# Kernel tuning notes

Measured on AMD Instinct MI355X. Metric: run time of the kernel, lower is better.

Reference implementation:

```python
import jax, jax.numpy as jnp
import numpy as np

B, N, C, K, D = 32, 4096, 37, 100, 512   # images, rois, classes(incl bg), max dets/class, feat dim
C1 = C - 1
SCORE_TH, NMS_TH = 0.1, 0.4
BBOX_STDS = jnp.array([0.1, 0.1, 0.2, 0.2], jnp.float32)
HS, WS, SCALE = 960.0, 1280.0, 1.6  # scaled image height/width, resize scale


def setup_inputs() -> dict:
    key = jax.random.key(0)
    k1, k2, k3, k4 = jax.random.split(key, 4)
    u = jax.random.uniform(k1, (B, N, 4))
    x1 = u[..., 0] * (WS - 160.0)
    y1 = u[..., 1] * (HS - 160.0)
    w = u[..., 2] * 140.0 + 20.0
    h = u[..., 3] * 140.0 + 20.0
    boxes = jnp.stack([x1, y1, x1 + w, y1 + h], -1)          # [B,N,4] in scaled coords
    box_deltas = jax.random.normal(k2, (B, N, 4 * C)) * 0.5   # [B,N,4C]
    scores = jax.nn.softmax(jax.random.normal(k3, (B, N, C)) * 2.0, axis=-1)  # [B,N,C]
    roi_features = jax.random.normal(k4, (B, N, D))           # [B,N,D]
    im_info = jnp.tile(jnp.array([[HS, WS, SCALE]], jnp.float32), (B, 1))     # [B,3]
    return dict(boxes=boxes, box_deltas=box_deltas, scores=scores,
                roi_features=roi_features, im_info=im_info)


def _decode_clip(boxes, deltas, im_info):
    # bbox_transform_inv with normalize stds, then clip_boxes, then /scale.
    d = deltas.reshape(B, N, C, 4) * BBOX_STDS                # [B,N,C,4]
    w = boxes[..., 2] - boxes[..., 0] + 1.0
    h = boxes[..., 3] - boxes[..., 1] + 1.0
    cx = boxes[..., 0] + 0.5 * w
    cy = boxes[..., 1] + 0.5 * h
    pcx = d[..., 0] * w[..., None] + cx[..., None]
    pcy = d[..., 1] * h[..., None] + cy[..., None]
    pw = jnp.exp(d[..., 2]) * w[..., None]
    ph = jnp.exp(d[..., 3]) * h[..., None]
    hmax = im_info[:, 0][:, None, None] - 1.0
    wmax = im_info[:, 1][:, None, None] - 1.0
    x1 = jnp.clip(pcx - 0.5 * pw, 0.0, wmax)
    y1 = jnp.clip(pcy - 0.5 * ph, 0.0, hmax)
    x2 = jnp.clip(pcx + 0.5 * pw, 0.0, wmax)
    y2 = jnp.clip(pcy + 0.5 * ph, 0.0, hmax)
    pred = jnp.stack([x1, y1, x2, y2], -1)                    # [B,N,C,4]
    return pred / im_info[:, 2][:, None, None, None]


def _pairwise_iou(b):
    # b: [K,4] -> [K,K]
    area = (b[:, 2] - b[:, 0]) * (b[:, 3] - b[:, 1])
    lt = jnp.maximum(b[:, None, :2], b[None, :, :2])
    rb = jnp.minimum(b[:, None, 2:], b[None, :, 2:])
    wh = jnp.clip(rb - lt, 0.0)
    inter = wh[..., 0] * wh[..., 1]
    return inter / (area[:, None] + area[None, :] - inter + 1e-8)


def _nms_one_class(cls_boxes, cls_scores, feats):
    # cls_boxes [N,4], cls_scores [N], feats [N,D] -> det [K, 4+1+D]
    s = jnp.where(cls_scores > SCORE_TH, cls_scores, -1.0)
    vals, idx = jax.lax.top_k(s, K)                           # sorted desc == torch.sort(desc)
    b = cls_boxes[idx]                                        # [K,4]
    ious = _pairwise_iou(b)                                   # [K,K]
    valid = vals > SCORE_TH
    rng = jnp.arange(K)

    def body(i, keep):
        sup = (ious[i] > NMS_TH) & (rng > i) & keep[i]
        return keep & ~sup

    keep = jax.lax.fori_loop(0, K, body, valid)               # greedy NMS, fixed size
    det = jnp.concatenate([b, vals[:, None], feats[idx]], -1)  # [K,5+D]
    return jnp.where(keep[:, None], det, 0.0)


def reference(boxes, box_deltas, scores, roi_features, im_info):
    pred = _decode_clip(boxes, box_deltas, im_info)           # [B,N,C,4]
    cls_boxes = pred[:, :, 1:, :]                             # drop background, [B,N,C1,4]
    cls_scores = scores[:, :, 1:]                             # [B,N,C1]
    per_image = jax.vmap(_nms_one_class, in_axes=(1, 1, None))  # over class axis
    per_batch = jax.vmap(per_image, in_axes=(0, 0, 0))          # over image axis
    return per_batch(cls_boxes, cls_scores, roi_features)     # [B,C1,K,5+D]
```

## Files before the change

### kernel.cpp

```cpp
#include <hip/hip_runtime.h>
#include <cmath>

#define BB 32
#define NN 4096
#define NC 37
#define C1 36
#define KK 100
#define DD 512
#define SCORE_TH 0.1f
#define NMS_TH 0.4f
#define NBC (BB * C1)
#define LCAP 2048
#define OCAP 2048
#define NT 256

__global__ __launch_bounds__(256) void transpose_kernel(
    const float* __restrict__ scores,
    float* __restrict__ scoresT)
{
    __shared__ float tile[37 * 65];

    const int b  = blockIdx.x >> 6;
    const int t0 = (blockIdx.x & 63) * 64;
    const int tid = threadIdx.x;

    const float4* src4 = (const float4*)(scores + ((size_t)b * NN + t0) * NC);
    for (int q = tid; q < (64 * 37) / 4; q += 256) {
        float4 v = src4[q];
        int e = q * 4;
        #pragma unroll
        for (int u = 0; u < 4; ++u) {
            int i = (e + u) / 37;
            int c = (e + u) - i * 37;
            float x = (u == 0) ? v.x : (u == 1) ? v.y : (u == 2) ? v.z : v.w;
            tile[c * 65 + i] = x;
        }
    }
    __syncthreads();

    float* dst = scoresT + (size_t)b * C1 * NN + t0;
    for (int q = tid; q < 36 * 16; q += 256) {
        int c1 = q >> 4;
        int i4 = (q & 15) * 4;
        float4 v;
        v.x = tile[(c1 + 1) * 65 + i4 + 0];
        v.y = tile[(c1 + 1) * 65 + i4 + 1];
        v.z = tile[(c1 + 1) * 65 + i4 + 2];
        v.w = tile[(c1 + 1) * 65 + i4 + 3];
        *(float4*)(dst + (size_t)c1 * NN + i4) = v;
    }
}

__global__ __launch_bounds__(NT) void detect_kernel(
    const float* __restrict__ boxes,
    const float* __restrict__ deltas,
    const float* __restrict__ feats,
    const float* __restrict__ im_info,
    const float* __restrict__ scoresT,
    unsigned long long* __restrict__ gover,
    float* __restrict__ out)
{
#pragma clang fp contract(off)
    __shared__ unsigned long long cand[LCAP];
    __shared__ int scnt;
    __shared__ float sbox[KK][4];
    __shared__ float sarea[KK];
    __shared__ float sval[KK];
    __shared__ int   sidx[KK];
    __shared__ int   skeep[KK];
    __shared__ unsigned int smeta[KK];

    const int bc  = blockIdx.x;
    const int b   = bc / C1;
    const int c   = bc % C1;
    const int tid = threadIdx.x;

    if (tid == 0) scnt = 0;
    __syncthreads();

    unsigned long long* over = gover + (size_t)bc * OCAP;
    const float4* s4 = (const float4*)(scoresT + (size_t)bc * NN);
    for (int i = tid; i < NN / 4; i += NT) {
        float4 v = s4[i];
        const int n0 = i * 4;
        #pragma unroll
        for (int u = 0; u < 4; ++u) {
            float x = (u == 0) ? v.x : (u == 1) ? v.y : (u == 2) ? v.z : v.w;
            if (x > SCORE_TH) {
                int pos = atomicAdd(&scnt, 1);
                unsigned long long key =
                    ((unsigned long long)__float_as_uint(x) << 32) |
                    (unsigned int)(0xFFFFFFFFu - (unsigned int)(n0 + u));
                if (pos < LCAP) cand[pos] = key;
                else            over[pos - LCAP] = key;
            }
        }
    }
    __syncthreads();
    const int M = scnt;

    int consumed = (M < LCAP) ? M : LCAP;
    int total    = consumed;
    for (;;) {
        int P = 128; while (P < total) P <<= 1;
        for (int i = total + tid; i < P; i += NT) cand[i] = 0ULL;
        __syncthreads();
        for (int k = 2; k <= P; k <<= 1) {
            for (int j = k >> 1; j > 0; j >>= 1) {
                for (int i = tid; i < P; i += NT) {
                    int ixj = i ^ j;
                    if (ixj > i) {
                        unsigned long long a  = cand[i];
                        unsigned long long bb = cand[ixj];
                        bool desc = ((i & k) == 0);
                        if (desc ? (a < bb) : (a > bb)) {
                            cand[i]   = bb;
                            cand[ixj] = a;
                        }
                    }
                }
                __syncthreads();
            }
        }
        if (consumed >= M) break;
        int t2 = M - consumed;
        if (t2 > LCAP - KK) t2 = LCAP - KK;
        for (int i = tid; i < t2; i += NT) cand[KK + i] = over[consumed - LCAP + i];
        consumed += t2;
        total = KK + t2;
        __syncthreads();
    }

    const int V = (M < KK) ? M : KK;

    if (tid < KK) {
        int k = tid;
        if (k < V) {
            unsigned long long key = cand[k];
            float v = __uint_as_float((unsigned int)(key >> 32));
            int   n = (int)(0xFFFFFFFFu - (unsigned int)(key & 0xFFFFFFFFull));
            sval[k] = v;
            sidx[k] = n;
            skeep[k] = 1;

            const float* bp = boxes + (b * NN + n) * 4;
            float bx1 = bp[0], by1 = bp[1], bx2 = bp[2], by2 = bp[3];
            const float* dp = deltas + ((b * NN + n) * NC + (c + 1)) * 4;
            float d0 = dp[0] * 0.1f;
            float d1 = dp[1] * 0.1f;
            float d2 = dp[2] * 0.2f;
            float d3 = dp[3] * 0.2f;

            float w  = bx2 - bx1 + 1.0f;
            float h  = by2 - by1 + 1.0f;
            float cx = bx1 + 0.5f * w;
            float cy = by1 + 0.5f * h;
            float pcx = d0 * w + cx;
            float pcy = d1 * h + cy;
            float pw  = (float)exp((double)d2) * w;
            float ph  = (float)exp((double)d3) * h;

            float hmax = im_info[b * 3 + 0] - 1.0f;
            float wmax = im_info[b * 3 + 1] - 1.0f;
            float sc   = im_info[b * 3 + 2];

            float x1p = fminf(fmaxf(pcx - 0.5f * pw, 0.0f), wmax);
            float y1p = fminf(fmaxf(pcy - 0.5f * ph, 0.0f), hmax);
            float x2p = fminf(fmaxf(pcx + 0.5f * pw, 0.0f), wmax);
            float y2p = fminf(fmaxf(pcy + 0.5f * ph, 0.0f), hmax);
            x1p = x1p / sc; y1p = y1p / sc; x2p = x2p / sc; y2p = y2p / sc;

            sbox[k][0] = x1p; sbox[k][1] = y1p; sbox[k][2] = x2p; sbox[k][3] = y2p;
            sarea[k] = (x2p - x1p) * (y2p - y1p);
        } else {
            sval[k] = 0.0f; sidx[k] = 0; skeep[k] = 0;
            sbox[k][0] = sbox[k][1] = sbox[k][2] = sbox[k][3] = 0.0f;
            sarea[k] = 0.0f;
        }
    }
    __syncthreads();

    if (tid < 64) {
        const int ln = tid;
        float ax1 = sbox[ln][0], ay1 = sbox[ln][1], ax2 = sbox[ln][2], ay2 = sbox[ln][3];
        float aar = sarea[ln];
        int   ka  = (ln < V) ? 1 : 0;
        float bx1 = 0.f, by1 = 0.f, bx2 = 0.f, by2 = 0.f, bar = 0.f;
        int   kb  = 0;
        if (ln < KK - 64) {
            bx1 = sbox[64 + ln][0]; by1 = sbox[64 + ln][1];
            bx2 = sbox[64 + ln][2]; by2 = sbox[64 + ln][3];
            bar = sarea[64 + ln];
            kb  = (64 + ln < V) ? 1 : 0;
        }
        for (int i = 0; i < V; ++i) {
            const int  srcl = i & 63;
            const bool hi   = (i >= 64);
            int ki = __shfl(hi ? kb : ka, srcl);
            if (ki) {
                float ix1 = __shfl(hi ? bx1 : ax1, srcl);
                float iy1 = __shfl(hi ? by1 : ay1, srcl);
                float ix2 = __shfl(hi ? bx2 : ax2, srcl);
                float iy2 = __shfl(hi ? by2 : ay2, srcl);
                float iar = __shfl(hi ? bar : aar, srcl);
                if (ka && ln > i) {
                    float ltx = fmaxf(ix1, ax1);
                    float lty = fmaxf(iy1, ay1);
                    float rbx = fminf(ix2, ax2);
                    float rby = fminf(iy2, ay2);
                    float iw = fmaxf(rbx - ltx, 0.0f);
                    float ih = fmaxf(rby - lty, 0.0f);
                    float inter = iw * ih;
                    float denom = iar + aar;
                    denom = denom - inter;
                    denom = denom + 1e-8f;
                    if (inter / denom > NMS_TH) ka = 0;
                }
                if (kb && 64 + ln > i) {
                    float ltx = fmaxf(ix1, bx1);
                    float lty = fmaxf(iy1, by1);
                    float rbx = fminf(ix2, bx2);
                    float rby = fminf(iy2, by2);
                    float iw = fmaxf(rbx - ltx, 0.0f);
                    float ih = fmaxf(rby - lty, 0.0f);
                    float inter = iw * ih;
                    float denom = iar + bar;
                    denom = denom - inter;
                    denom = denom + 1e-8f;
                    if (inter / denom > NMS_TH) kb = 0;
                }
            }
        }
        skeep[ln] = ka;
        if (ln < KK - 64) skeep[64 + ln] = kb;
    }
    __syncthreads();

    const long long bcbase = (long long)bc * (KK * 517);
    for (int e = tid; e < KK; e += NT)
        smeta[e] = skeep[e] ? (0x80000000u | (unsigned)sidx[e]) : 0u;
    for (int e = tid; e < KK * 5; e += NT) {
        int k = e / 5, j = e - k * 5;
        float hv = (j < 4) ? sbox[k][j] : sval[k];
        if (!skeep[k]) hv = 0.0f;
        out[bcbase + (long long)k * 517 + j] = hv;
    }
    __syncthreads();

    const int wv = tid >> 6;
    const int ln = tid & 63;
    const int k0 = wv * 25;
    int mym = (ln < 25) ? (int)smeta[k0 + ln] : 0;
    const float* fbase = feats + (long long)b * NN * DD;
#pragma unroll 2
    for (int t = 0; t < 25; ++t) {
        unsigned int m = (unsigned int)__shfl(mym, t);
        const int  n  = (int)(m & 0x7FFFFFFFu);
        const bool kp = (m & 0x80000000u) != 0u;
        const float* fp = fbase + (long long)n * DD + ln;
        float v0 = fp[0];
        float v1 = fp[64];
        float v2 = fp[128];
        float v3 = fp[192];
        float v4 = fp[256];
        float v5 = fp[320];
        float v6 = fp[384];
        float v7 = fp[448];
        if (!kp) { v0 = v1 = v2 = v3 = v4 = v5 = v6 = v7 = 0.0f; }
        float* op = out + bcbase + (long long)(k0 + t) * 517 + 5 + ln;
        __builtin_nontemporal_store(v0, op + 0);
        __builtin_nontemporal_store(v1, op + 64);
        __builtin_nontemporal_store(v2, op + 128);
        __builtin_nontemporal_store(v3, op + 192);
        __builtin_nontemporal_store(v4, op + 256);
        __builtin_nontemporal_store(v5, op + 320);
        __builtin_nontemporal_store(v6, op + 384);
        __builtin_nontemporal_store(v7, op + 448);
    }
}

extern "C" void kernel_launch(void* const* d_in, const int* in_sizes, int n_in,
                              void* d_out, int out_size, void* d_ws, size_t ws_size,
                              hipStream_t stream) {
    const float* boxes    = (const float*)d_in[0];
    const float* deltas   = (const float*)d_in[1];
    const float* scores   = (const float*)d_in[2];
    const float* feats    = (const float*)d_in[3];
    const float* im_info  = (const float*)d_in[4];
    float* out = (float*)d_out;

    char* ws = (char*)d_ws;
    float* scoresT = (float*)ws;
    unsigned long long* gover =
        (unsigned long long*)(ws + (size_t)NBC * NN * sizeof(float));

    transpose_kernel<<<dim3(BB * 64), dim3(256), 0, stream>>>(scores, scoresT);
    detect_kernel<<<dim3(NBC), dim3(NT), 0, stream>>>(
        boxes, deltas, feats, im_info, scoresT, gover, out);
}
```

Before: 538.2 us.

## Split feature gather into a separate emit kernel with row-parallel grid

Moves the per-detection feature gather out of the NMS kernel into a new emit kernel that launches one wave per two output rows across all images and classes. Kept indices are passed through a workspace metadata array. This is meant to free the gather from the 1152-block, latency-bound NMS kernel so the large output write can use many more waves in flight. It costs an extra launch and a small global round-trip of metadata, and assumes the workspace is big enough for the new array.

```diff
diff --git a/kernel.cpp b/kernel.cpp
--- a/kernel.cpp
+++ b/kernel.cpp
@@ -10,6 +10,7 @@
 #define SCORE_TH 0.1f
 #define NMS_TH 0.4f
 #define NBC (BB * C1)
+#define NROWS (NBC * KK)
 #define LCAP 2048
 #define OCAP 2048
 #define NT 256
@@ -51,13 +52,13 @@
     }
 }
 
-__global__ __launch_bounds__(NT) void detect_kernel(
+__global__ __launch_bounds__(NT) void select_kernel(
     const float* __restrict__ boxes,
     const float* __restrict__ deltas,
-    const float* __restrict__ feats,
     const float* __restrict__ im_info,
     const float* __restrict__ scoresT,
     unsigned long long* __restrict__ gover,
+    unsigned int* __restrict__ meta,
     float* __restrict__ out)
 {
 #pragma clang fp contract(off)
@@ -68,7 +69,6 @@
     __shared__ float sval[KK];
     __shared__ int   sidx[KK];
     __shared__ int   skeep[KK];
-    __shared__ unsigned int smeta[KK];
 
     const int bc  = blockIdx.x;
     const int b   = bc / C1;
@@ -238,45 +238,60 @@
 
     const long long bcbase = (long long)bc * (KK * 517);
     for (int e = tid; e < KK; e += NT)
-        smeta[e] = skeep[e] ? (0x80000000u | (unsigned)sidx[e]) : 0u;
+        meta[bc * KK + e] = skeep[e] ? (0x80000000u | (unsigned)sidx[e]) : 0u;
     for (int e = tid; e < KK * 5; e += NT) {
         int k = e / 5, j = e - k * 5;
         float hv = (j < 4) ? sbox[k][j] : sval[k];
         if (!skeep[k]) hv = 0.0f;
         out[bcbase + (long long)k * 517 + j] = hv;
     }
-    __syncthreads();
-
-    const int wv = tid >> 6;
-    const int ln = tid & 63;
-    const int k0 = wv * 25;
-    int mym = (ln < 25) ? (int)smeta[k0 + ln] : 0;
-    const float* fbase = feats + (long long)b * NN * DD;
-#pragma unroll 2
-    for (int t = 0; t < 25; ++t) {
-        unsigned int m = (unsigned int)__shfl(mym, t);
-        const int  n  = (int)(m & 0x7FFFFFFFu);
-        const bool kp = (m & 0x80000000u) != 0u;
-        const float* fp = fbase + (long long)n * DD + ln;
-        float v0 = fp[0];
-        float v1 = fp[64];
-        float v2 = fp[128];
-        float v3 = fp[192];
-        float v4 = fp[256];
-        float v5 = fp[320];
-        float v6 = fp[384];
-        float v7 = fp[448];
-        if (!kp) { v0 = v1 = v2 = v3 = v4 = v5 = v6 = v7 = 0.0f; }
-        float* op = out + bcbase + (long long)(k0 + t) * 517 + 5 + ln;
-        __builtin_nontemporal_store(v0, op + 0);
-        __builtin_nontemporal_store(v1, op + 64);
-        __builtin_nontemporal_store(v2, op + 128);
-        __builtin_nontemporal_store(v3, op + 192);
-        __builtin_nontemporal_store(v4, op + 256);
-        __builtin_nontemporal_store(v5, op + 320);
-        __builtin_nontemporal_store(v6, op + 384);
-        __builtin_nontemporal_store(v7, op + 448);
-    }
+}
+
+__global__ __launch_bounds__(256) void emit_kernel(
+    const float* __restrict__ feats,
+    const unsigned int* __restrict__ meta,
+    float* __restrict__ out)
+{
+    const int wv = threadIdx.x >> 6;
+    const int ln = threadIdx.x & 63;
+    const int r0 = blockIdx.x * 8 + wv * 2;
+
+    const unsigned m0 = meta[r0];
+    const unsigned m1 = meta[r0 + 1];
+    const int b0 = r0 / (C1 * KK);
+    const int b1 = (r0 + 1) / (C1 * KK);
+    const long long n0 = (long long)(m0 & 0x7FFFFFFFu);
+    const long long n1 = (long long)(m1 & 0x7FFFFFFFu);
+
+    const float* fp0 = feats + ((long long)b0 * NN + n0) * DD + ln;
+    const float* fp1 = feats + ((long long)b1 * NN + n1) * DD + ln;
+
+    float a0 = fp0[0],   a1 = fp0[64],  a2 = fp0[128], a3 = fp0[192];
+    float a4 = fp0[256], a5 = fp0[320], a6 = fp0[384], a7 = fp0[448];
+    float c0 = fp1[0],   c1 = fp1[64],  c2 = fp1[128], c3 = fp1[192];
+    float c4 = fp1[256], c5 = fp1[320], c6 = fp1[384], c7 = fp1[448];
+
+    if (!(m0 & 0x80000000u)) { a0=a1=a2=a3=a4=a5=a6=a7=0.0f; }
+    if (!(m1 & 0x80000000u)) { c0=c1=c2=c3=c4=c5=c6=c7=0.0f; }
+
+    float* o0 = out + (long long)r0 * 517 + 5 + ln;
+    float* o1 = o0 + 517;
+    __builtin_nontemporal_store(a0, o0 + 0);
+    __builtin_nontemporal_store(a1, o0 + 64);
+    __builtin_nontemporal_store(a2, o0 + 128);
+    __builtin_nontemporal_store(a3, o0 + 192);
+    __builtin_nontemporal_store(a4, o0 + 256);
+    __builtin_nontemporal_store(a5, o0 + 320);
+    __builtin_nontemporal_store(a6, o0 + 384);
+    __builtin_nontemporal_store(a7, o0 + 448);
+    __builtin_nontemporal_store(c0, o1 + 0);
+    __builtin_nontemporal_store(c1, o1 + 64);
+    __builtin_nontemporal_store(c2, o1 + 128);
+    __builtin_nontemporal_store(c3, o1 + 192);
+    __builtin_nontemporal_store(c4, o1 + 256);
+    __builtin_nontemporal_store(c5, o1 + 320);
+    __builtin_nontemporal_store(c6, o1 + 384);
+    __builtin_nontemporal_store(c7, o1 + 448);
 }
 
 extern "C" void kernel_launch(void* const* d_in, const int* in_sizes, int n_in,
@@ -293,8 +308,12 @@
     float* scoresT = (float*)ws;
     unsigned long long* gover =
         (unsigned long long*)(ws + (size_t)NBC * NN * sizeof(float));
+    unsigned int* meta =
+        (unsigned int*)(ws + (size_t)NBC * NN * sizeof(float)
+                           + (size_t)NBC * OCAP * sizeof(unsigned long long));
 
     transpose_kernel<<<dim3(BB * 64), dim3(256), 0, stream>>>(scores, scoresT);
-    detect_kernel<<<dim3(NBC), dim3(NT), 0, stream>>>(
-        boxes, deltas, feats, im_info, scoresT, gover, out);
+    select_kernel<<<dim3(NBC), dim3(NT), 0, stream>>>(
+        boxes, deltas, im_info, scoresT, gover, meta, out);
+    emit_kernel<<<dim3(NROWS / 8), dim3(256), 0, stream>>>(feats, meta, out);
 }
```

Result: no change. 544.2 us (+1.1%).
